# Kernel optimization log

Measured on AMD Instinct MI355X. Metric: run time of the kernel, lower is better.

Reference implementation:

```python
import jax, jax.numpy as jnp
import numpy as np

NUM_GRAPHS = 64

def _sage(x, edge_index, Wl, bl, Wr):
    # PyG SAGEConv (mean aggr): out = lin_l(mean_{j in N(i)} x_j) + lin_r(x_i)
    src, dst = edge_index[0], edge_index[1]
    n = x.shape[0]
    summed = jax.ops.segment_sum(x[src], dst, num_segments=n)        # [N,F]
    deg = jax.ops.segment_sum(jnp.ones_like(src, dtype=x.dtype), dst, num_segments=n)
    agg = summed / jnp.maximum(deg, 1.0)[:, None]
    return agg @ Wl.T + bl + x @ Wr.T

def setup_inputs() -> dict:
    key = jax.random.key(0)
    ks = jax.random.split(key, 12)
    N, E, F, H = 50000, 600000, 128, 128
    x = jax.random.normal(ks[0], (N, F), dtype=jnp.float32)
    edge_index = jax.random.randint(ks[1], (2, E), 0, N, dtype=jnp.int64)
    batch = jnp.sort(jax.random.randint(ks[2], (N,), 0, NUM_GRAPHS, dtype=jnp.int64))
    s = lambda fan_in: 1.0 / np.sqrt(fan_in)
    return {
        "x": x, "edge_index": edge_index, "batch": batch,
        "W1l": jax.random.uniform(ks[3], (H, F), minval=-s(F), maxval=s(F)),
        "b1l": jnp.zeros((H,), jnp.float32),
        "W1r": jax.random.uniform(ks[4], (H, F), minval=-s(F), maxval=s(F)),
        "W2l": jax.random.uniform(ks[5], (H, H), minval=-s(H), maxval=s(H)),
        "b2l": jnp.zeros((H,), jnp.float32),
        "W2r": jax.random.uniform(ks[6], (H, H), minval=-s(H), maxval=s(H)),
        "Wc1": jax.random.uniform(ks[7], (H, H), minval=-s(H), maxval=s(H)),
        "bc1": jax.random.uniform(ks[8], (H,), minval=-s(H), maxval=s(H)),
        "Wc2": jax.random.uniform(ks[9], (1, H), minval=-s(H), maxval=s(H)),
        "bc2": jax.random.uniform(ks[10], (1,), minval=-s(H), maxval=s(H)),
    }

def reference(x, edge_index, batch, W1l, b1l, W1r, W2l, b2l, W2r, Wc1, bc1, Wc2, bc2):
    h = jax.nn.relu(_sage(x, edge_index, W1l, b1l, W1r))
    h = jax.nn.relu(_sage(h, edge_index, W2l, b2l, W2r))
    # global mean pool per graph
    gsum = jax.ops.segment_sum(h, batch, num_segments=NUM_GRAPHS)
    gcnt = jax.ops.segment_sum(jnp.ones((h.shape[0],), h.dtype), batch, num_segments=NUM_GRAPHS)
    gemb = gsum / jnp.maximum(gcnt, 1.0)[:, None]                    # [G,H]
    # classifier MLP (dropout = identity in eval)
    z = jax.nn.relu(gemb @ Wc1.T + bc1)
    out = (z @ Wc2.T + bc2).squeeze(-1)                              # [G]
    return out
```

## Files before the change

kernel.cpp:

```cpp
#include <hip/hip_runtime.h>


typedef __attribute__((ext_vector_type(8))) short bf16x8;
typedef __attribute__((ext_vector_type(8))) unsigned short ushort8;
typedef __attribute__((ext_vector_type(4))) float f32x4;

#define HBLK 4096

__device__ inline unsigned short f2bf(float f) {
  unsigned u = __float_as_uint(f);
  u += 0x7fff + ((u >> 16) & 1);
  return (unsigned short)(u >> 16);
}
__device__ inline float bf2f(unsigned short h) { return __uint_as_float(((unsigned)h) << 16); }


__global__ __launch_bounds__(256) void k_hist(const int* __restrict__ ei, int* __restrict__ bhist, int E) {
  __shared__ int h[256];
  int tid = threadIdx.x;
  h[tid] = 0;
  __syncthreads();
  int base = blockIdx.x * HBLK;
  int end = min(base + HBLK, E);
  for (int e = base + tid; e < end; e += 256) {
    int d = ei[E + e];
    atomicAdd(&h[d >> 8], 1);
  }
  __syncthreads();
  bhist[blockIdx.x * 256 + tid] = h[tid];
}

__global__ __launch_bounds__(256) void k_bscan_a(const int* __restrict__ bhist, int* __restrict__ bukbase,
                                                 int nblk) {
  __shared__ int s[256];
  int t = threadIdx.x;
  int sum = 0;
  for (int b = 0; b < nblk; ++b) sum += bhist[b * 256 + t];
  s[t] = sum;
  __syncthreads();
  for (int d = 1; d < 256; d <<= 1) {
    int v = (t >= d) ? s[t - d] : 0;
    __syncthreads();
    s[t] += v;
    __syncthreads();
  }
  bukbase[t] = s[t] - sum;
  if (t == 255) bukbase[256] = s[255];
}

__global__ __launch_bounds__(256) void k_bscan_b(int* __restrict__ bhist, const int* __restrict__ bukbase,
                                                 int nblk) {
  __shared__ int s[256];
  int buk = blockIdx.x;
  int t = threadIdx.x;
  int c = (t < nblk) ? bhist[t * 256 + buk] : 0;
  s[t] = c;
  __syncthreads();
  for (int d = 1; d < 256; d <<= 1) {
    int v = (t >= d) ? s[t - d] : 0;
    __syncthreads();
    s[t] += v;
    __syncthreads();
  }
  if (t < nblk) bhist[t * 256 + buk] = bukbase[buk] + s[t] - c;
}

__global__ __launch_bounds__(256) void k_scat(const int* __restrict__ ei, const int* __restrict__ bhist,
                                              unsigned* __restrict__ ebuk, int E) {
  __shared__ int cur[256];
  int tid = threadIdx.x;
  cur[tid] = bhist[blockIdx.x * 256 + tid];
  __syncthreads();
  int base = blockIdx.x * HBLK;
  int end = min(base + HBLK, E);
  for (int e = base + tid; e < end; e += 256) {
    int d = ei[E + e];
    int srcv = ei[e];
    int p = atomicAdd(&cur[d >> 8], 1);
    ebuk[p] = ((unsigned)(d & 255) << 24) | (unsigned)srcv;
  }
}

__global__ __launch_bounds__(256) void k_bucket(const unsigned* __restrict__ ebuk,
                                                const int* __restrict__ bukbase,
                                                int* __restrict__ off, int* __restrict__ colv,
                                                int N, int E) {
  __shared__ int h[256];
  __shared__ int cur[256];
  __shared__ int sc[256];
  int tid = threadIdx.x;
  int buk = blockIdx.x;
  int b0 = bukbase[buk], b1 = bukbase[buk + 1];
  h[tid] = 0;
  __syncthreads();
  for (int i = b0 + tid; i < b1; i += 256) atomicAdd(&h[ebuk[i] >> 24], 1);
  __syncthreads();
  int my = h[tid];
  sc[tid] = my;
  __syncthreads();
  for (int d = 1; d < 256; d <<= 1) {
    int v = (tid >= d) ? sc[tid - d] : 0;
    __syncthreads();
    sc[tid] += v;
    __syncthreads();
  }
  int excl = sc[tid] - my;
  cur[tid] = excl;
  int node = buk * 256 + tid;
  if (node < N) off[node] = b0 + excl;
  if (buk == gridDim.x - 1 && tid == 0) off[N] = E;
  __syncthreads();
  for (int i = b0 + tid; i < b1; i += 256) {
    unsigned v = ebuk[i];
    int p = atomicAdd(&cur[v >> 24], 1);
    colv[b0 + p] = (int)(v & 0xFFFFFFu);
  }
}


__global__ __launch_bounds__(64) void k_gcnt_bs(const int* __restrict__ batch, int* __restrict__ gcnt,
                                                int N, int G) {
  int g = threadIdx.x;
  if (g >= G) return;
  int lo = 0, hi = N;
  while (lo < hi) { int mid = (lo + hi) >> 1; if (batch[mid] < g) lo = mid + 1; else hi = mid; }
  int a = lo;
  lo = 0; hi = N;
  while (lo < hi) { int mid = (lo + hi) >> 1; if (batch[mid] < g + 1) lo = mid + 1; else hi = mid; }
  gcnt[g] = lo - a;
}


__global__ __launch_bounds__(256) void k_tobf(const float* __restrict__ x,
                                              unsigned short* __restrict__ xbf, int total) {
  int i = (blockIdx.x * 256 + threadIdx.x) * 4;
  if (i + 3 < total) {
    float4 v = *(const float4*)(x + i);
    ushort4 p;
    p.x = f2bf(v.x); p.y = f2bf(v.y); p.z = f2bf(v.z); p.w = f2bf(v.w);
    *(ushort4*)(xbf + i) = p;
  } else {
    for (int k = 0; k < 4 && i + k < total; ++k) xbf[i + k] = f2bf(x[i + k]);
  }
}


__global__ __launch_bounds__(256) void k_agg_bf(const unsigned short* __restrict__ Xbf,
                                                const int* __restrict__ off, const int* __restrict__ col,
                                                float* __restrict__ T, int N) {
  int wid = (blockIdx.x * 256 + threadIdx.x) >> 6;
  int ln = threadIdx.x & 63;
  if (wid >= N) return;
  int o0 = off[wid], o1 = off[wid + 1];
  int deg = o1 - o0;
  int rs = ln >> 4, fs = ln & 15;
  float acc[8];
#pragma unroll
  for (int j = 0; j < 8; ++j) acc[j] = 0.f;

  for (int base = 0; base < deg; base += 16) {
#pragma unroll
    for (int u = 0; u < 4; ++u) {
      int n = base + u * 4 + rs;
      if (n < deg) {
        int idx = col[o0 + n];
        ushort8 q = *(const ushort8*)(Xbf + (size_t)idx * 128 + fs * 8);
#pragma unroll
        for (int j = 0; j < 8; ++j) acc[j] += bf2f(q[j]);
      }
    }
  }
#pragma unroll
  for (int j = 0; j < 8; ++j) {
    acc[j] += __shfl_xor(acc[j], 16);
    acc[j] += __shfl_xor(acc[j], 32);
  }
  if (rs == 0) {
    float sc = 1.0f / (float)max(deg, 1);
    float4 r0 = {acc[0] * sc, acc[1] * sc, acc[2] * sc, acc[3] * sc};
    float4 r1 = {acc[4] * sc, acc[5] * sc, acc[6] * sc, acc[7] * sc};
    *(float4*)(T + (size_t)wid * 128 + fs * 8) = r0;
    *(float4*)(T + (size_t)wid * 128 + fs * 8 + 4) = r1;
  }
}


__global__ __launch_bounds__(256) void k_wprep(const float* __restrict__ Wl, const float* __restrict__ Wr,
                                               unsigned short* __restrict__ Bpre) {
  int id = blockIdx.x * 256 + threadIdx.x;
  if (id >= 4096) return;
  int kk = id >> 9;
  int ct = (id >> 6) & 7;
  int l  = id & 63;
  int colIdx = ct * 16 + (l & 15);
  int k0 = kk * 32 + (l >> 4) * 8;
  const float* W = (k0 < 128) ? Wl : Wr;
  int kb = k0 & 127;
#pragma unroll
  for (int j = 0; j < 8; ++j) {
    float v = W[colIdx * 128 + kb + j];
    unsigned short h = f2bf(v);
    size_t bh = (size_t)kk * 8192 + ((size_t)ct * 64 + l) * 8 + j;
    Bpre[bh] = h;
    Bpre[bh + 4096] = f2bf(v - bf2f(h));
  }
}


__global__ __launch_bounds__(256) void k_lin_mfma(
    const float* __restrict__ A,
    const float* __restrict__ Xf,
    const unsigned short* __restrict__ Xbf,
    const unsigned short* __restrict__ Bpre,
    const float* __restrict__ bias,
    unsigned short* __restrict__ OUTbf,
    const int* __restrict__ batch, float* __restrict__ gsum,
    int N, int mode) {
  __shared__ unsigned short As[4096];
  __shared__ unsigned short Bs[8192];
  __shared__ float ps[128];

  int tid = threadIdx.x;
  int wv = tid >> 6, ln = tid & 63;
  int rowBase = blockIdx.x * 64;

  int sRow = tid >> 2;
  int sKq = tid & 3;
  int sgr = min(rowBase + sRow, N - 1);
  int sSlot = ((sRow >> 4) * 64 + (sKq << 4) + (sRow & 15)) * 8;

  f32x4 acc[4][2];
#pragma unroll
  for (int rg = 0; rg < 4; ++rg) {
    acc[rg][0] = (f32x4){0.f, 0.f, 0.f, 0.f};
    acc[rg][1] = (f32x4){0.f, 0.f, 0.f, 0.f};
  }

  const uint4* BpreV = (const uint4*)Bpre;

  for (int kk = 0; kk < 8; ++kk) {
    bool selfTerm = (kk >= 4);
    int kOff = (kk & 3) * 32 + sKq * 8;
    uint4 b0 = BpreV[kk * 1024 + tid];
    uint4 b1 = BpreV[kk * 1024 + tid + 256];
    uint4 b2 = BpreV[kk * 1024 + tid + 512];
    uint4 b3 = BpreV[kk * 1024 + tid + 768];

    uint4 uh, ul;
    bool bf16Self = selfTerm && (mode == 1);
    if (bf16Self) {
      uh = *(const uint4*)(Xbf + (size_t)sgr * 128 + kOff);
      ul = (uint4){0u, 0u, 0u, 0u};
    } else {
      const float* S = selfTerm ? Xf : A;
      float4 p0 = *(const float4*)(S + (size_t)sgr * 128 + kOff);
      float4 p1 = *(const float4*)(S + (size_t)sgr * 128 + kOff + 4);
      float fv[8] = {p0.x, p0.y, p0.z, p0.w, p1.x, p1.y, p1.z, p1.w};
      unsigned short hh[8], ll[8];
#pragma unroll
      for (int j = 0; j < 8; ++j) {
        unsigned short h = f2bf(fv[j]);
        hh[j] = h;
        ll[j] = f2bf(fv[j] - bf2f(h));
      }
      uh.x = (unsigned)hh[0] | ((unsigned)hh[1] << 16);
      uh.y = (unsigned)hh[2] | ((unsigned)hh[3] << 16);
      uh.z = (unsigned)hh[4] | ((unsigned)hh[5] << 16);
      uh.w = (unsigned)hh[6] | ((unsigned)hh[7] << 16);
      ul.x = (unsigned)ll[0] | ((unsigned)ll[1] << 16);
      ul.y = (unsigned)ll[2] | ((unsigned)ll[3] << 16);
      ul.z = (unsigned)ll[4] | ((unsigned)ll[5] << 16);
      ul.w = (unsigned)ll[6] | ((unsigned)ll[7] << 16);
    }

    __syncthreads();
    *(uint4*)(As + sSlot) = uh;
    *(uint4*)(As + 2048 + sSlot) = ul;
    uint4* BsV = (uint4*)Bs;
    BsV[tid] = b0;
    BsV[tid + 256] = b1;
    BsV[tid + 512] = b2;
    BsV[tid + 768] = b3;
    __syncthreads();

    int c0 = wv * 2;
    bf16x8 bh0 = *(bf16x8*)(Bs + ((size_t)c0 * 64 + ln) * 8);
    bf16x8 bl0 = *(bf16x8*)(Bs + 4096 + ((size_t)c0 * 64 + ln) * 8);
    bf16x8 bh1 = *(bf16x8*)(Bs + ((size_t)(c0 + 1) * 64 + ln) * 8);
    bf16x8 bl1 = *(bf16x8*)(Bs + 4096 + ((size_t)(c0 + 1) * 64 + ln) * 8);
    bool doLo = !bf16Self;
#pragma unroll
    for (int rg = 0; rg < 4; ++rg) {
      bf16x8 ah = *(bf16x8*)(As + ((size_t)rg * 64 + ln) * 8);
      bf16x8 al = *(bf16x8*)(As + 2048 + ((size_t)rg * 64 + ln) * 8);
      acc[rg][0] = __builtin_amdgcn_mfma_f32_16x16x32_bf16(ah, bh0, acc[rg][0], 0, 0, 0);
      acc[rg][0] = __builtin_amdgcn_mfma_f32_16x16x32_bf16(ah, bl0, acc[rg][0], 0, 0, 0);
      acc[rg][1] = __builtin_amdgcn_mfma_f32_16x16x32_bf16(ah, bh1, acc[rg][1], 0, 0, 0);
      acc[rg][1] = __builtin_amdgcn_mfma_f32_16x16x32_bf16(ah, bl1, acc[rg][1], 0, 0, 0);
      if (doLo) {
        acc[rg][0] = __builtin_amdgcn_mfma_f32_16x16x32_bf16(al, bh0, acc[rg][0], 0, 0, 0);
        acc[rg][1] = __builtin_amdgcn_mfma_f32_16x16x32_bf16(al, bh1, acc[rg][1], 0, 0, 0);
      }
    }
  }

  int lcol = ln & 15;
  int rsub = (ln >> 4) * 4;
#pragma unroll
  for (int c = 0; c < 2; ++c) {
    float b = bias[(wv * 2 + c) * 16 + lcol];
#pragma unroll
    for (int rg = 0; rg < 4; ++rg)
#pragma unroll
      for (int r = 0; r < 4; ++r) acc[rg][c][r] = fmaxf(acc[rg][c][r] + b, 0.f);
  }

  if (mode == 0) {
#pragma unroll
    for (int rg = 0; rg < 4; ++rg)
#pragma unroll
      for (int r = 0; r < 4; ++r) {
        int row = rowBase + rg * 16 + rsub + r;
        if (row < N) {
          OUTbf[(size_t)row * 128 + (wv * 2 + 0) * 16 + lcol] = f2bf(acc[rg][0][r]);
          OUTbf[(size_t)row * 128 + (wv * 2 + 1) * 16 + lcol] = f2bf(acc[rg][1][r]);
        }
      }
  } else {
    if (tid < 128) ps[tid] = 0.f;
    __syncthreads();
    int lastRow = min(rowBase + 63, N - 1);
    int g0 = batch[rowBase], g1 = batch[lastRow];
    if (g0 == g1) {
#pragma unroll
      for (int c = 0; c < 2; ++c) {
        float s = 0.f;
#pragma unroll
        for (int rg = 0; rg < 4; ++rg)
#pragma unroll
          for (int r = 0; r < 4; ++r) {
            int row = rowBase + rg * 16 + rsub + r;
            if (row < N) s += acc[rg][c][r];
          }
        atomicAdd(&ps[(wv * 2 + c) * 16 + lcol], s);
      }
      __syncthreads();
      if (tid < 128) atomicAdd(&gsum[g0 * 128 + tid], ps[tid]);
    } else {
#pragma unroll
      for (int rg = 0; rg < 4; ++rg)
#pragma unroll
        for (int r = 0; r < 4; ++r) {
          int row = rowBase + rg * 16 + rsub + r;
          if (row < N) {
            int g = batch[row];
            atomicAdd(&gsum[g * 128 + (wv * 2 + 0) * 16 + lcol], acc[rg][0][r]);
            atomicAdd(&gsum[g * 128 + (wv * 2 + 1) * 16 + lcol], acc[rg][1][r]);
          }
        }
    }
  }
}


__global__ __launch_bounds__(128) void k_cls1(const float* __restrict__ gsum, const int* __restrict__ gcnt,
                                              const float* __restrict__ Wc1, const float* __restrict__ bc1,
                                              float* __restrict__ z) {
  int g = blockIdx.x;
  int h = threadIdx.x;
  float inv = 1.0f / (float)max(gcnt[g], 1);
  float s = 0.f;
  for (int f = 0; f < 128; ++f) s += gsum[g * 128 + f] * Wc1[h * 128 + f];
  z[g * 128 + h] = fmaxf(s * inv + bc1[h], 0.f);
}

__global__ __launch_bounds__(128) void k_cls2(const float* __restrict__ z, const float* __restrict__ Wc2,
                                              const float* __restrict__ bc2, float* __restrict__ out) {
  __shared__ float red[128];
  int g = blockIdx.x;
  int t = threadIdx.x;
  red[t] = z[g * 128 + t] * Wc2[t];
  __syncthreads();
  for (int d = 64; d > 0; d >>= 1) {
    if (t < d) red[t] += red[t + d];
    __syncthreads();
  }
  if (t == 0) out[g] = red[0] + bc2[0];
}


extern "C" void kernel_launch(void* const* d_in, const int* in_sizes, int n_in,
                              void* d_out, int out_size, void* d_ws, size_t ws_size,
                              hipStream_t stream) {
  const float* x   = (const float*)d_in[0];
  const int*   ei  = (const int*)d_in[1];
  const int*   bat = (const int*)d_in[2];
  const float* W1l = (const float*)d_in[3];
  const float* b1l = (const float*)d_in[4];
  const float* W1r = (const float*)d_in[5];
  const float* W2l = (const float*)d_in[6];
  const float* b2l = (const float*)d_in[7];
  const float* W2r = (const float*)d_in[8];
  const float* Wc1 = (const float*)d_in[9];
  const float* bc1 = (const float*)d_in[10];
  const float* Wc2 = (const float*)d_in[11];
  const float* bc2 = (const float*)d_in[12];
  float* out = (float*)d_out;

  int N = in_sizes[0] / 128;
  int E = in_sizes[1] / 2;
  int nEblk = (E + HBLK - 1) / HBLK;
  int nBuk = (N + 255) >> 8;

  char* ws = (char*)d_ws;
  size_t o = 0;
  auto alloc = [&](size_t bytes) {
    char* p = ws + o;
    o += (bytes + 255) & ~(size_t)255;
    return p;
  };
  int*      off    = (int*)alloc((size_t)(N + 1) * 4);
  int*      col    = (int*)alloc((size_t)E * 4);
  unsigned* ebuk   = (unsigned*)alloc((size_t)E * 4);
  int*      bhist  = (int*)alloc((size_t)nEblk * 256 * 4);
  int*      bukbase= (int*)alloc(257 * 4);
  float*    T      = (float*)alloc((size_t)N * 128 * 4);
  unsigned short* xbf  = (unsigned short*)alloc((size_t)N * 128 * 2);
  unsigned short* h1bf = (unsigned short*)alloc((size_t)N * 128 * 2);
  unsigned short* Bpre1 = (unsigned short*)alloc(65536 * 2);
  unsigned short* Bpre2 = (unsigned short*)alloc(65536 * 2);
  float*    gsum   = (float*)alloc(64 * 128 * 4 + 64 * 4);
  int*      gcnt   = (int*)(gsum + 64 * 128);
  float*    z      = (float*)alloc(64 * 128 * 4);

  hipMemsetAsync(gsum, 0, 64 * 128 * 4, stream);

  k_tobf<<<(N * 128 / 4 + 255) / 256, 256, 0, stream>>>(x, xbf, N * 128);
  k_wprep<<<16, 256, 0, stream>>>(W1l, W1r, Bpre1);
  k_wprep<<<16, 256, 0, stream>>>(W2l, W2r, Bpre2);
  k_gcnt_bs<<<1, 64, 0, stream>>>(bat, gcnt, N, 64);

  k_hist<<<nEblk, 256, 0, stream>>>(ei, bhist, E);
  k_bscan_a<<<1, 256, 0, stream>>>(bhist, bukbase, nEblk);
  k_bscan_b<<<256, 256, 0, stream>>>(bhist, bukbase, nEblk);
  k_scat<<<nEblk, 256, 0, stream>>>(ei, bhist, ebuk, E);
  k_bucket<<<nBuk, 256, 0, stream>>>(ebuk, bukbase, off, col, N, E);

  int nLinBlk = (N + 63) / 64;
  k_agg_bf<<<(N + 3) / 4, 256, 0, stream>>>(xbf, off, col, T, N);
  k_lin_mfma<<<nLinBlk, 256, 0, stream>>>(T, x, nullptr, Bpre1, b1l, h1bf, bat, gsum, N, 0);
  k_agg_bf<<<(N + 3) / 4, 256, 0, stream>>>(h1bf, off, col, T, N);
  k_lin_mfma<<<nLinBlk, 256, 0, stream>>>(T, nullptr, h1bf, Bpre2, b2l, nullptr, bat, gsum, N, 1);

  k_cls1<<<64, 128, 0, stream>>>(gsum, gcnt, Wc1, bc1, z);
  k_cls2<<<64, 128, 0, stream>>>(z, Wc2, bc2, out);
}
```

Before: 191.6 us.

## Merge prep kernels, store aggregates in bf16, fuse classifier kernels

Five setup launches (bf16 conversion, two weight preps, degree histogram, graph counts) plus the gsum memset become one multi-role kernel dispatched by block index. The aggregation output T is now written as bf16 instead of fp32, which halves its traffic, and the linear layer drops the low-part split and MFMAs for the aggregate term. The two classifier kernels are fused into one. The bf16 aggregate lowers precision of the neighbour-mean term compared with the previous hi/lo split.

```diff
diff --git a/kernel.cpp b/kernel.cpp
--- a/kernel.cpp
+++ b/kernel.cpp
@@ -15,20 +15,73 @@
 __device__ inline float bf2f(unsigned short h) { return __uint_as_float(((unsigned)h) << 16); }
 
 
-__global__ __launch_bounds__(256) void k_hist(const int* __restrict__ ei, int* __restrict__ bhist, int E) {
+__device__ inline void wprep_body(int id, const float* __restrict__ Wl, const float* __restrict__ Wr,
+                                  unsigned short* __restrict__ Bpre) {
+  if (id >= 4096) return;
+  int kk = id >> 9;
+  int ct = (id >> 6) & 7;
+  int l  = id & 63;
+  int colIdx = ct * 16 + (l & 15);
+  int k0 = kk * 32 + (l >> 4) * 8;
+  const float* W = (k0 < 128) ? Wl : Wr;
+  int kb = k0 & 127;
+#pragma unroll
+  for (int j = 0; j < 8; ++j) {
+    float v = W[colIdx * 128 + kb + j];
+    unsigned short h = f2bf(v);
+    size_t bh = (size_t)kk * 8192 + ((size_t)ct * 64 + l) * 8 + j;
+    Bpre[bh] = h;
+    Bpre[bh + 4096] = f2bf(v - bf2f(h));
+  }
+}
+
+__global__ __launch_bounds__(256) void k_prep(
+    const float* __restrict__ x, unsigned short* __restrict__ xbf, int total,
+    const float* __restrict__ W1l, const float* __restrict__ W1r, unsigned short* __restrict__ Bpre1,
+    const float* __restrict__ W2l, const float* __restrict__ W2r, unsigned short* __restrict__ Bpre2,
+    const int* __restrict__ batch, int* __restrict__ gcnt, float* __restrict__ gsum, int N,
+    const int* __restrict__ ei, int* __restrict__ bhist, int E,
+    int nTobf, int nEblk) {
   __shared__ int h[256];
+  int b = blockIdx.x;
   int tid = threadIdx.x;
-  h[tid] = 0;
-  __syncthreads();
-  int base = blockIdx.x * HBLK;
-  int end = min(base + HBLK, E);
-  for (int e = base + tid; e < end; e += 256) {
-    int d = ei[E + e];
-    atomicAdd(&h[d >> 8], 1);
-  }
-  __syncthreads();
-  bhist[blockIdx.x * 256 + tid] = h[tid];
-}
+  if (b < nTobf) {
+    int i = (b * 256 + tid) * 4;
+    if (i + 3 < total) {
+      float4 v = *(const float4*)(x + i);
+      ushort4 p;
+      p.x = f2bf(v.x); p.y = f2bf(v.y); p.z = f2bf(v.z); p.w = f2bf(v.w);
+      *(ushort4*)(xbf + i) = p;
+    } else {
+      for (int k = 0; k < 4 && i + k < total; ++k) xbf[i + k] = f2bf(x[i + k]);
+    }
+  } else if (b < nTobf + 16) {
+    wprep_body((b - nTobf) * 256 + tid, W1l, W1r, Bpre1);
+  } else if (b < nTobf + 32) {
+    wprep_body((b - nTobf - 16) * 256 + tid, W2l, W2r, Bpre2);
+  } else if (b < nTobf + 32 + nEblk) {
+    int eb = b - nTobf - 32;
+    h[tid] = 0;
+    __syncthreads();
+    int base = eb * HBLK;
+    int end = min(base + HBLK, E);
+    for (int e = base + tid; e < end; e += 256) atomicAdd(&h[ei[E + e] >> 8], 1);
+    __syncthreads();
+    bhist[eb * 256 + tid] = h[tid];
+  } else {
+    for (int i = tid; i < 64 * 128; i += 256) gsum[i] = 0.f;
+    if (tid < 64) {
+      int g = tid;
+      int lo = 0, hi = N;
+      while (lo < hi) { int mid = (lo + hi) >> 1; if (batch[mid] < g) lo = mid + 1; else hi = mid; }
+      int a = lo;
+      lo = 0; hi = N;
+      while (lo < hi) { int mid = (lo + hi) >> 1; if (batch[mid] < g + 1) lo = mid + 1; else hi = mid; }
+      gcnt[g] = lo - a;
+    }
+  }
+}
+
 
 __global__ __launch_bounds__(256) void k_bscan_a(const int* __restrict__ bhist, int* __restrict__ bukbase,
                                                  int nblk) {
@@ -118,36 +171,9 @@
 }
 
 
-__global__ __launch_bounds__(64) void k_gcnt_bs(const int* __restrict__ batch, int* __restrict__ gcnt,
-                                                int N, int G) {
-  int g = threadIdx.x;
-  if (g >= G) return;
-  int lo = 0, hi = N;
-  while (lo < hi) { int mid = (lo + hi) >> 1; if (batch[mid] < g) lo = mid + 1; else hi = mid; }
-  int a = lo;
-  lo = 0; hi = N;
-  while (lo < hi) { int mid = (lo + hi) >> 1; if (batch[mid] < g + 1) lo = mid + 1; else hi = mid; }
-  gcnt[g] = lo - a;
-}
-
-
-__global__ __launch_bounds__(256) void k_tobf(const float* __restrict__ x,
-                                              unsigned short* __restrict__ xbf, int total) {
-  int i = (blockIdx.x * 256 + threadIdx.x) * 4;
-  if (i + 3 < total) {
-    float4 v = *(const float4*)(x + i);
-    ushort4 p;
-    p.x = f2bf(v.x); p.y = f2bf(v.y); p.z = f2bf(v.z); p.w = f2bf(v.w);
-    *(ushort4*)(xbf + i) = p;
-  } else {
-    for (int k = 0; k < 4 && i + k < total; ++k) xbf[i + k] = f2bf(x[i + k]);
-  }
-}
-
-
 __global__ __launch_bounds__(256) void k_agg_bf(const unsigned short* __restrict__ Xbf,
                                                 const int* __restrict__ off, const int* __restrict__ col,
-                                                float* __restrict__ T, int N) {
+                                                unsigned short* __restrict__ Tbf, int N) {
   int wid = (blockIdx.x * 256 + threadIdx.x) >> 6;
   int ln = threadIdx.x & 63;
   if (wid >= N) return;
@@ -177,38 +203,21 @@
   }
   if (rs == 0) {
     float sc = 1.0f / (float)max(deg, 1);
-    float4 r0 = {acc[0] * sc, acc[1] * sc, acc[2] * sc, acc[3] * sc};
-    float4 r1 = {acc[4] * sc, acc[5] * sc, acc[6] * sc, acc[7] * sc};
-    *(float4*)(T + (size_t)wid * 128 + fs * 8) = r0;
-    *(float4*)(T + (size_t)wid * 128 + fs * 8 + 4) = r1;
-  }
-}
-
-
-__global__ __launch_bounds__(256) void k_wprep(const float* __restrict__ Wl, const float* __restrict__ Wr,
-                                               unsigned short* __restrict__ Bpre) {
-  int id = blockIdx.x * 256 + threadIdx.x;
-  if (id >= 4096) return;
-  int kk = id >> 9;
-  int ct = (id >> 6) & 7;
-  int l  = id & 63;
-  int colIdx = ct * 16 + (l & 15);
-  int k0 = kk * 32 + (l >> 4) * 8;
-  const float* W = (k0 < 128) ? Wl : Wr;
-  int kb = k0 & 127;
-#pragma unroll
-  for (int j = 0; j < 8; ++j) {
-    float v = W[colIdx * 128 + kb + j];
-    unsigned short h = f2bf(v);
-    size_t bh = (size_t)kk * 8192 + ((size_t)ct * 64 + l) * 8 + j;
-    Bpre[bh] = h;
-    Bpre[bh + 4096] = f2bf(v - bf2f(h));
+    unsigned short w[8];
+#pragma unroll
+    for (int j = 0; j < 8; ++j) w[j] = f2bf(acc[j] * sc);
+    uint4 uw;
+    uw.x = (unsigned)w[0] | ((unsigned)w[1] << 16);
+    uw.y = (unsigned)w[2] | ((unsigned)w[3] << 16);
+    uw.z = (unsigned)w[4] | ((unsigned)w[5] << 16);
+    uw.w = (unsigned)w[6] | ((unsigned)w[7] << 16);
+    *(uint4*)(Tbf + (size_t)wid * 128 + fs * 8) = uw;
   }
 }
 
 
 __global__ __launch_bounds__(256) void k_lin_mfma(
-    const float* __restrict__ A,
+    const unsigned short* __restrict__ Tbf,
     const float* __restrict__ Xf,
     const unsigned short* __restrict__ Xbf,
     const unsigned short* __restrict__ Bpre,
@@ -246,15 +255,15 @@
     uint4 b2 = BpreV[kk * 1024 + tid + 512];
     uint4 b3 = BpreV[kk * 1024 + tid + 768];
 
-    uint4 uh, ul;
-    bool bf16Self = selfTerm && (mode == 1);
-    if (bf16Self) {
+    uint4 uh = {0u, 0u, 0u, 0u}, ul = {0u, 0u, 0u, 0u};
+    bool doLo = selfTerm && (mode == 0);
+    if (!selfTerm) {
+      uh = *(const uint4*)(Tbf + (size_t)sgr * 128 + kOff);
+    } else if (mode == 1) {
       uh = *(const uint4*)(Xbf + (size_t)sgr * 128 + kOff);
-      ul = (uint4){0u, 0u, 0u, 0u};
     } else {
-      const float* S = selfTerm ? Xf : A;
-      float4 p0 = *(const float4*)(S + (size_t)sgr * 128 + kOff);
-      float4 p1 = *(const float4*)(S + (size_t)sgr * 128 + kOff + 4);
+      float4 p0 = *(const float4*)(Xf + (size_t)sgr * 128 + kOff);
+      float4 p1 = *(const float4*)(Xf + (size_t)sgr * 128 + kOff + 4);
       float fv[8] = {p0.x, p0.y, p0.z, p0.w, p1.x, p1.y, p1.z, p1.w};
       unsigned short hh[8], ll[8];
 #pragma unroll
@@ -275,7 +284,7 @@
 
     __syncthreads();
     *(uint4*)(As + sSlot) = uh;
-    *(uint4*)(As + 2048 + sSlot) = ul;
+    if (doLo) *(uint4*)(As + 2048 + sSlot) = ul;
     uint4* BsV = (uint4*)Bs;
     BsV[tid] = b0;
     BsV[tid + 256] = b1;
@@ -288,16 +297,15 @@
     bf16x8 bl0 = *(bf16x8*)(Bs + 4096 + ((size_t)c0 * 64 + ln) * 8);
     bf16x8 bh1 = *(bf16x8*)(Bs + ((size_t)(c0 + 1) * 64 + ln) * 8);
     bf16x8 bl1 = *(bf16x8*)(Bs + 4096 + ((size_t)(c0 + 1) * 64 + ln) * 8);
-    bool doLo = !bf16Self;
 #pragma unroll
     for (int rg = 0; rg < 4; ++rg) {
       bf16x8 ah = *(bf16x8*)(As + ((size_t)rg * 64 + ln) * 8);
-      bf16x8 al = *(bf16x8*)(As + 2048 + ((size_t)rg * 64 + ln) * 8);
       acc[rg][0] = __builtin_amdgcn_mfma_f32_16x16x32_bf16(ah, bh0, acc[rg][0], 0, 0, 0);
       acc[rg][0] = __builtin_amdgcn_mfma_f32_16x16x32_bf16(ah, bl0, acc[rg][0], 0, 0, 0);
       acc[rg][1] = __builtin_amdgcn_mfma_f32_16x16x32_bf16(ah, bh1, acc[rg][1], 0, 0, 0);
       acc[rg][1] = __builtin_amdgcn_mfma_f32_16x16x32_bf16(ah, bl1, acc[rg][1], 0, 0, 0);
       if (doLo) {
+        bf16x8 al = *(bf16x8*)(As + 2048 + ((size_t)rg * 64 + ln) * 8);
         acc[rg][0] = __builtin_amdgcn_mfma_f32_16x16x32_bf16(al, bh0, acc[rg][0], 0, 0, 0);
         acc[rg][1] = __builtin_amdgcn_mfma_f32_16x16x32_bf16(al, bh1, acc[rg][1], 0, 0, 0);
       }
@@ -363,29 +371,23 @@
 }
 
 
-__global__ __launch_bounds__(128) void k_cls1(const float* __restrict__ gsum, const int* __restrict__ gcnt,
-                                              const float* __restrict__ Wc1, const float* __restrict__ bc1,
-                                              float* __restrict__ z) {
+__global__ __launch_bounds__(128) void k_cls(const float* __restrict__ gsum, const int* __restrict__ gcnt,
+                                             const float* __restrict__ Wc1, const float* __restrict__ bc1,
+                                             const float* __restrict__ Wc2, const float* __restrict__ bc2,
+                                             float* __restrict__ out) {
+  __shared__ float red[128];
   int g = blockIdx.x;
   int h = threadIdx.x;
   float inv = 1.0f / (float)max(gcnt[g], 1);
   float s = 0.f;
   for (int f = 0; f < 128; ++f) s += gsum[g * 128 + f] * Wc1[h * 128 + f];
-  z[g * 128 + h] = fmaxf(s * inv + bc1[h], 0.f);
-}
-
-__global__ __launch_bounds__(128) void k_cls2(const float* __restrict__ z, const float* __restrict__ Wc2,
-                                              const float* __restrict__ bc2, float* __restrict__ out) {
-  __shared__ float red[128];
-  int g = blockIdx.x;
-  int t = threadIdx.x;
-  red[t] = z[g * 128 + t] * Wc2[t];
+  red[h] = fmaxf(s * inv + bc1[h], 0.f) * Wc2[h];
   __syncthreads();
   for (int d = 64; d > 0; d >>= 1) {
-    if (t < d) red[t] += red[t + d];
-    __syncthreads();
-  }
-  if (t == 0) out[g] = red[0] + bc2[0];
+    if (h < d) red[h] += red[h + d];
+    __syncthreads();
+  }
+  if (h == 0) out[g] = red[0] + bc2[0];
 }
 
 
@@ -411,6 +413,8 @@
   int E = in_sizes[1] / 2;
   int nEblk = (E + HBLK - 1) / HBLK;
   int nBuk = (N + 255) >> 8;
+  int total = N * 128;
+  int nTobf = (total / 4 + 255) / 256;
 
   char* ws = (char*)d_ws;
   size_t o = 0;
@@ -424,34 +428,28 @@
   unsigned* ebuk   = (unsigned*)alloc((size_t)E * 4);
   int*      bhist  = (int*)alloc((size_t)nEblk * 256 * 4);
   int*      bukbase= (int*)alloc(257 * 4);
-  float*    T      = (float*)alloc((size_t)N * 128 * 4);
+  unsigned short* Tbf  = (unsigned short*)alloc((size_t)N * 128 * 2);
   unsigned short* xbf  = (unsigned short*)alloc((size_t)N * 128 * 2);
   unsigned short* h1bf = (unsigned short*)alloc((size_t)N * 128 * 2);
   unsigned short* Bpre1 = (unsigned short*)alloc(65536 * 2);
   unsigned short* Bpre2 = (unsigned short*)alloc(65536 * 2);
   float*    gsum   = (float*)alloc(64 * 128 * 4 + 64 * 4);
   int*      gcnt   = (int*)(gsum + 64 * 128);
-  float*    z      = (float*)alloc(64 * 128 * 4);
-
-  hipMemsetAsync(gsum, 0, 64 * 128 * 4, stream);
-
-  k_tobf<<<(N * 128 / 4 + 255) / 256, 256, 0, stream>>>(x, xbf, N * 128);
-  k_wprep<<<16, 256, 0, stream>>>(W1l, W1r, Bpre1);
-  k_wprep<<<16, 256, 0, stream>>>(W2l, W2r, Bpre2);
-  k_gcnt_bs<<<1, 64, 0, stream>>>(bat, gcnt, N, 64);
-
-  k_hist<<<nEblk, 256, 0, stream>>>(ei, bhist, E);
+
+  k_prep<<<nTobf + 32 + nEblk + 1, 256, 0, stream>>>(
+      x, xbf, total, W1l, W1r, Bpre1, W2l, W2r, Bpre2,
+      bat, gcnt, gsum, N, ei, bhist, E, nTobf, nEblk);
+
   k_bscan_a<<<1, 256, 0, stream>>>(bhist, bukbase, nEblk);
   k_bscan_b<<<256, 256, 0, stream>>>(bhist, bukbase, nEblk);
   k_scat<<<nEblk, 256, 0, stream>>>(ei, bhist, ebuk, E);
   k_bucket<<<nBuk, 256, 0, stream>>>(ebuk, bukbase, off, col, N, E);
 
   int nLinBlk = (N + 63) / 64;
-  k_agg_bf<<<(N + 3) / 4, 256, 0, stream>>>(xbf, off, col, T, N);
-  k_lin_mfma<<<nLinBlk, 256, 0, stream>>>(T, x, nullptr, Bpre1, b1l, h1bf, bat, gsum, N, 0);
-  k_agg_bf<<<(N + 3) / 4, 256, 0, stream>>>(h1bf, off, col, T, N);
-  k_lin_mfma<<<nLinBlk, 256, 0, stream>>>(T, nullptr, h1bf, Bpre2, b2l, nullptr, bat, gsum, N, 1);
-
-  k_cls1<<<64, 128, 0, stream>>>(gsum, gcnt, Wc1, bc1, z);
-  k_cls2<<<64, 128, 0, stream>>>(z, Wc2, bc2, out);
-}
+  k_agg_bf<<<(N + 3) / 4, 256, 0, stream>>>(xbf, off, col, Tbf, N);
+  k_lin_mfma<<<nLinBlk, 256, 0, stream>>>(Tbf, x, nullptr, Bpre1, b1l, h1bf, bat, gsum, N, 0);
+  k_agg_bf<<<(N + 3) / 4, 256, 0, stream>>>(h1bf, off, col, Tbf, N);
+  k_lin_mfma<<<nLinBlk, 256, 0, stream>>>(Tbf, nullptr, h1bf, Bpre2, b2l, nullptr, bat, gsum, N, 1);
+
+  k_cls<<<64, 128, 0, stream>>>(gsum, gcnt, Wc1, bc1, Wc2, bc2, out);
+}
```

New measurement: 168.5 us. -12.0%, faster.
